# Optimization experiments

Hardware: AMD Instinct MI355X
Metric: run time of the kernel (lower is better)

## Reference

```python
import jax, jax.numpy as jnp
import numpy as np

D_MODEL, D_K, D_V, NUM_HEADS = 1024, 64, 64, 16
B, T = 4, 2048


def setup_inputs() -> dict:
    key = jax.random.key(0)
    ks = jax.random.split(key, 9)
    s = 0.02
    inp = {
        "input_Q": jax.random.normal(ks[0], (B, T, D_MODEL), dtype=jnp.float32),
        # causal mask: True = masked out (matches torch masked_fill semantics)
        "mask": jnp.triu(jnp.ones((T, T), dtype=bool), k=1),
        "Wq": jax.random.normal(ks[1], (D_MODEL, D_K * NUM_HEADS), dtype=jnp.float32) * s,
        "bq": jnp.zeros((D_K * NUM_HEADS,), dtype=jnp.float32),
        "Wk": jax.random.normal(ks[2], (D_MODEL, D_K * NUM_HEADS), dtype=jnp.float32) * s,
        "bk": jnp.zeros((D_K * NUM_HEADS,), dtype=jnp.float32),
        "Wv": jax.random.normal(ks[3], (D_MODEL, D_V * NUM_HEADS), dtype=jnp.float32) * s,
        "bv": jnp.zeros((D_V * NUM_HEADS,), dtype=jnp.float32),
        "Wo": jax.random.normal(ks[4], (D_V * NUM_HEADS, D_MODEL), dtype=jnp.float32) * s,
        "bo": jnp.zeros((D_MODEL,), dtype=jnp.float32),
    }
    return inp


def reference(input_Q, mask, Wq, bq, Wk, bk, Wv, bv, Wo, bo):
    b, t, _ = input_Q.shape
    h, dk, dv = NUM_HEADS, D_K, D_V
    # projections, then split heads: [b, t, h*d] -> [b, h, t, d]
    Q = (input_Q @ Wq + bq).reshape(b, t, h, dk).transpose(0, 2, 1, 3)
    K = (input_Q @ Wk + bk).reshape(b, t, h, dk).transpose(0, 2, 1, 3)
    V = (input_Q @ Wv + bv).reshape(b, t, h, dv).transpose(0, 2, 1, 3)
    # scaled dot-product attention with full [b, h, t, t] scores (as original)
    scores = jnp.einsum("bhqd,bhkd->bhqk", Q, K) * (1.0 / np.sqrt(dk).astype(np.float32))
    scores = jnp.where(mask, jnp.float32(-jnp.inf), scores)
    attn = jax.nn.softmax(scores, axis=-1)
    ctx = jnp.einsum("bhqk,bhkd->bhqd", attn, V)  # [b, h, t, dv]
    combined = ctx.transpose(0, 2, 1, 3).reshape(b, t, h * dv)
    return combined @ Wo + bo
```

## Files before the change

### kernel.cpp

```cpp
#include <hip/hip_runtime.h>
#include <hip/hip_bf16.h>
#include <stdint.h>

#define B_  4
#define T_  2048
#define H_  16
#define DH  64
#define DM  1024

typedef unsigned short u16;
typedef float  f32x4  __attribute__((ext_vector_type(4)));
typedef u16    u16x4  __attribute__((ext_vector_type(4)));
typedef __bf16 bf16x8 __attribute__((ext_vector_type(8)));
typedef bf16x8 __attribute__((may_alias, aligned(16))) bf16x8_a;
typedef u16x4  __attribute__((may_alias, aligned(8)))  u16x4_a;

__device__ __forceinline__ void gld16(void* lds, const void* g) {
  __builtin_amdgcn_global_load_lds((const __attribute__((address_space(1))) unsigned int*)g,
                                   (__attribute__((address_space(3))) unsigned int*)lds,
                                   16, 0, 0);
}
__device__ __forceinline__ u16 f2b(float f) {
  __bf16 h = (__bf16)f; return __builtin_bit_cast(unsigned short, h);
}

__global__ void cvt_x(const float* __restrict__ in, u16* __restrict__ out) {
  const int i = (blockIdx.x * 256 + threadIdx.x) * 4;
  const f32x4 v = *(const f32x4*)&in[i];
  u16x4 o;
  o.x = f2b(v.x); o.y = f2b(v.y); o.z = f2b(v.z); o.w = f2b(v.w);
  *(u16x4_a*)&out[i] = o;
}

__global__ void transpose4(const float* __restrict__ Wq, const float* __restrict__ Wk,
                           const float* __restrict__ Wv, const float* __restrict__ Wo,
                           u16* __restrict__ WqT, u16* __restrict__ WkT,
                           u16* __restrict__ WvT, u16* __restrict__ WoT) {
  const float* in; u16* out;
  switch (blockIdx.z) {
    case 0: in = Wq; out = WqT; break;
    case 1: in = Wk; out = WkT; break;
    case 2: in = Wv; out = WvT; break;
    default: in = Wo; out = WoT; break;
  }
  __shared__ u16 t[32][33];
  const int bx = blockIdx.x * 32, by = blockIdx.y * 32;
  const int tx = threadIdx.x & 31, ty = threadIdx.x >> 5;
  for (int i = ty; i < 32; i += 8) t[i][tx] = f2b(in[(size_t)(by + i) * DM + bx + tx]);
  __syncthreads();
  for (int i = ty; i < 32; i += 8) out[(size_t)(bx + i) * DM + by + tx] = t[tx][i];
}

__global__ void transpose_v(const u16* __restrict__ in, u16* __restrict__ out) {
  __shared__ u16 t[64][65];
  const int bh = blockIdx.y, t0 = blockIdx.x * 64;
  const int tx = threadIdx.x & 63, ty = threadIdx.x >> 6;
  const u16* ib = in  + (size_t)bh * T_ * DH;
  u16*       ob = out + (size_t)bh * DH * T_;
  for (int i = ty; i < 64; i += 4) t[i][tx] = ib[(size_t)(t0 + i) * DH + tx];
  __syncthreads();
  for (int i = ty; i < 64; i += 4) ob[(size_t)i * T_ + t0 + tx] = t[tx][i];
}

__device__ __forceinline__ void gemm_bt_128(
    const u16* __restrict__ A, const u16* __restrict__ BT,
    const float* __restrict__ bias, float oscale,
    u16* __restrict__ C, float* __restrict__ Cf, int mode)
{
  constexpr int K = 1024, N = 1024;
  __shared__ __attribute__((aligned(16))) u16 lA[128 * 32];
  __shared__ __attribute__((aligned(16))) u16 lB[128 * 32];
  const int tid  = threadIdx.x;
  const int lane = tid & 63;
  const int quad = lane >> 4, ln = lane & 15;
  const int wave = tid >> 6;
  const int wm = wave >> 1, wn = wave & 1;
  const int m0 = blockIdx.y * 128, n0 = blockIdx.x * 128;

  const f32x4 fz = {0.f, 0.f, 0.f, 0.f};
  f32x4 acc[4][4];
#pragma unroll
  for (int i = 0; i < 4; i++)
#pragma unroll
    for (int j = 0; j < 4; j++) acc[i][j] = fz;

  const int o0 = tid * 16;
  for (int k0 = 0; k0 < K; k0 += 32) {
    __syncthreads();
#pragma unroll
    for (int p = 0; p < 2; ++p) {
      const int o = p * 4096 + o0;
      const int row = o >> 6, cole = (o & 63) >> 1;
      gld16(&lA[o >> 1], &A [(size_t)(m0 + row) * K + k0 + cole]);
      gld16(&lB[o >> 1], &BT[(size_t)(n0 + row) * K + k0 + cole]);
    }
    __syncthreads();
    bf16x8 af[4], bf[4];
#pragma unroll
    for (int i = 0; i < 4; i++)
      af[i] = *(const bf16x8_a*)&lA[(wm * 64 + i * 16 + ln) * 32 + quad * 8];
#pragma unroll
    for (int j = 0; j < 4; j++)
      bf[j] = *(const bf16x8_a*)&lB[(wn * 64 + j * 16 + ln) * 32 + quad * 8];
#pragma unroll
    for (int i = 0; i < 4; i++)
#pragma unroll
      for (int j = 0; j < 4; j++)
        acc[i][j] = __builtin_amdgcn_mfma_f32_16x16x32_bf16(af[i], bf[j], acc[i][j], 0, 0, 0);
  }

#pragma unroll
  for (int j = 0; j < 4; j++) {
    const int n = n0 + wn * 64 + j * 16 + ln;
    const float bn = bias[n];
#pragma unroll
    for (int i = 0; i < 4; i++) {
      const int mb = m0 + wm * 64 + i * 16 + quad * 4;
#pragma unroll
      for (int r = 0; r < 4; r++) {
        const int m = mb + r;
        const float v = (acc[i][j][r] + bn) * oscale;
        if (mode == 0) {
          const int b = m >> 11, t = m & 2047, h = n >> 6, d = n & 63;
          C[((size_t)((b * H_ + h) * T_ + t)) * DH + d] = f2b(v);
        } else {
          Cf[(size_t)m * N + n] = v;
        }
      }
    }
  }
}

__global__ __launch_bounds__(256, 2) void qkv_gemm(
    const u16* __restrict__ X,
    const u16* __restrict__ WqT, const u16* __restrict__ WkT, const u16* __restrict__ WvT,
    const float* __restrict__ bq, const float* __restrict__ bk, const float* __restrict__ bv,
    u16* __restrict__ Qo, u16* __restrict__ Ko, u16* __restrict__ Vo)
{
  const u16 *BT; const float* bias; u16* C; float sc;
  if (blockIdx.z == 0)      { BT = WqT; bias = bq; C = Qo; sc = 0.1803368801111144f; }
  else if (blockIdx.z == 1) { BT = WkT; bias = bk; C = Ko; sc = 1.0f; }
  else                      { BT = WvT; bias = bv; C = Vo; sc = 1.0f; }
  gemm_bt_128(X, BT, bias, sc, C, nullptr, 0);
}

__global__ __launch_bounds__(256, 2) void out_gemm(
    const u16* __restrict__ ctx, const u16* __restrict__ WoT,
    const float* __restrict__ bo, float* __restrict__ out)
{
  gemm_bt_128(ctx, WoT, bo, 1.0f, nullptr, out, 2);
}

__global__ __launch_bounds__(512, 4) void flash_attn(
    const u16* __restrict__ Q, const u16* __restrict__ Kg,
    const u16* __restrict__ Vt, u16* __restrict__ ctx)
{
  __shared__ __attribute__((aligned(16))) u16 lK[128 * 64];
  __shared__ __attribute__((aligned(16))) u16 lV[64 * 128];
  __shared__ __attribute__((aligned(16))) u16 lP[128 * 64];

  const int bh = blockIdx.x;
  const int b  = bh >> 4, h = bh & 15;
  const int qi = 15 - blockIdx.y;
  const int q0 = qi * 128;
  const int tid = threadIdx.x;
  const int lane = tid & 63, wave = tid >> 6;
  const int quad = lane >> 4, ln = lane & 15;
  const int ln7 = ln & 7, ln8 = ln >> 3;
  const int w16 = wave * 16;

  const u16* Qbh = Q  + (size_t)bh * T_ * DH;
  const u16* Kbh = Kg + (size_t)bh * T_ * DH;
  const u16* Vbh = Vt + (size_t)bh * DH * T_;

#pragma unroll
  for (int p = 0; p < 2; ++p) {
    const int P = p * 512 + tid;
    const int row = P >> 3, c = (P & 7) ^ (row & 7);
    gld16(&lK[P * 8], &Qbh[(size_t)(q0 + row) * DH + c * 8]);
  }
  __syncthreads();
  bf16x8 aq[2];
#pragma unroll
  for (int ks = 0; ks < 2; ++ks)
    aq[ks] = *(const bf16x8_a*)&lK[(w16 + ln) * 64 + (((ks * 4 + quad) ^ ln7) << 3)];

  bf16x8 ones;
#pragma unroll
  for (int i = 0; i < 8; i++) ones[i] = (__bf16)1.0f;

  const f32x4 fz = {0.f, 0.f, 0.f, 0.f};
  f32x4 accO[4];
  f32x4 accL;
#pragma unroll
  for (int j = 0; j < 4; j++) accO[j] = fz;
  accL = fz;

  auto tile_step = [&](int kt, bool MASK) {
    const int t0 = kt * 128;
    __syncthreads();
#pragma unroll
    for (int p = 0; p < 2; ++p) {
      const int P = p * 512 + tid;
      const int row = P >> 3, c = (P & 7) ^ (row & 7);
      gld16(&lK[P * 8], &Kbh[(size_t)(t0 + row) * DH + c * 8]);
    }
#pragma unroll
    for (int p = 0; p < 2; ++p) {
      const int P = p * 512 + tid;
      const int row = P >> 4, c = (P & 15) ^ (row & 15);
      gld16(&lV[P * 8], &Vbh[(size_t)row * T_ + t0 + c * 8]);
    }
    __syncthreads();

#pragma unroll
    for (int half = 0; half < 2; ++half) {
      f32x4 s[4];
#pragma unroll
      for (int jj = 0; jj < 4; jj++) s[jj] = fz;
#pragma unroll
      for (int ks = 0; ks < 2; ++ks) {
        bf16x8 bk4[4];
#pragma unroll
        for (int jj = 0; jj < 4; jj++)
          bk4[jj] = *(const bf16x8_a*)&lK[((half * 4 + jj) * 16 + ln) * 64 + (((ks * 4 + quad) ^ ln7) << 3)];
#pragma unroll
        for (int jj = 0; jj < 4; jj++)
          s[jj] = __builtin_amdgcn_mfma_f32_16x16x32_bf16(aq[ks], bk4[jj], s[jj], 0, 0, 0);
      }

#pragma unroll
      for (int jj = 0; jj < 4; jj++)
#pragma unroll
        for (int r = 0; r < 4; r++) {
          float z = s[jj][r];
          if (MASK) {
            const int qrow = q0 + w16 + quad * 4 + r;
            if ((t0 + (half * 4 + jj) * 16 + ln) > qrow) z = -INFINITY;
          }
          s[jj][r] = __builtin_amdgcn_exp2f(z);
        }

#pragma unroll
      for (int jj = 0; jj < 4; jj++) {
        const int c = jj * 2 + ln8;
#pragma unroll
        for (int r = 0; r < 4; r++) {
          const int row = w16 + quad * 4 + r;
          lP[row * 64 + ((c ^ (row & 7)) << 3) + ln7] = f2b(s[jj][r]);
        }
      }

#pragma unroll
      for (int ks2 = 0; ks2 < 2; ++ks2) {
        const int ks = half * 2 + ks2;
        bf16x8 ap, bv4[4];
        ap = *(const bf16x8_a*)&lP[(w16 + ln) * 64 + (((ks2 * 4 + quad) ^ ln7) << 3)];
        accL = __builtin_amdgcn_mfma_f32_16x16x32_bf16(ap, ones, accL, 0, 0, 0);
#pragma unroll
        for (int j2 = 0; j2 < 4; j2++)
          bv4[j2] = *(const bf16x8_a*)&lV[(j2 * 16 + ln) * 128 + (((ks * 4 + quad) ^ ln) << 3)];
#pragma unroll
        for (int j2 = 0; j2 < 4; j2++)
          accO[j2] = __builtin_amdgcn_mfma_f32_16x16x32_bf16(ap, bv4[j2], accO[j2], 0, 0, 0);
      }
    }
  };

  for (int kt = 0; kt < qi; ++kt) tile_step(kt, false);
  tile_step(qi, true);

#pragma unroll
  for (int r = 0; r < 4; r++) {
    const int qrow = q0 + w16 + quad * 4 + r;
    const float inv = 1.0f / accL[r];
#pragma unroll
    for (int j2 = 0; j2 < 4; j2++) {
      const int d = j2 * 16 + ln;
      ctx[((size_t)(b * T_ + qrow)) * DM + h * DH + d] = f2b(accO[j2][r] * inv);
    }
  }
}

extern "C" void kernel_launch(void* const* d_in, const int* in_sizes, int n_in,
                              void* d_out, int out_size, void* d_ws, size_t ws_size,
                              hipStream_t stream) {
  (void)in_sizes; (void)n_in; (void)out_size; (void)ws_size;
  const float* X  = (const float*)d_in[0];
  const float* Wq = (const float*)d_in[2];
  const float* bq = (const float*)d_in[3];
  const float* Wk = (const float*)d_in[4];
  const float* bk = (const float*)d_in[5];
  const float* Wv = (const float*)d_in[6];
  const float* bv = (const float*)d_in[7];
  const float* Wo = (const float*)d_in[8];
  const float* bo = (const float*)d_in[9];
  float* out = (float*)d_out;

  char* ws = (char*)d_ws;
  u16* WqT = (u16*)(ws + (0ull  << 20));
  u16* WkT = (u16*)(ws + (2ull  << 20));
  u16* WvT = (u16*)(ws + (4ull  << 20));
  u16* WoT = (u16*)(ws + (6ull  << 20));
  u16* Xb  = (u16*)(ws + (8ull  << 20));
  u16* Qb  = (u16*)(ws + (24ull << 20));
  u16* Kb  = (u16*)(ws + (40ull << 20));
  u16* Vb  = (u16*)(ws + (56ull << 20));
  u16* Vtb = (u16*)(ws + (72ull << 20));
  u16* ctx = (u16*)(ws + (88ull << 20));

  cvt_x<<<8192, 256, 0, stream>>>(X, Xb);
  transpose4<<<dim3(32, 32, 4), 256, 0, stream>>>(Wq, Wk, Wv, Wo, WqT, WkT, WvT, WoT);
  qkv_gemm<<<dim3(8, 64, 3), 256, 0, stream>>>(Xb, WqT, WkT, WvT, bq, bk, bv, Qb, Kb, Vb);
  transpose_v<<<dim3(32, 64), 256, 0, stream>>>(Vb, Vtb);
  flash_attn<<<dim3(64, 16), 512, 0, stream>>>(Qb, Kb, Vtb, ctx);
  out_gemm<<<dim3(8, 64), 256, 0, stream>>>(ctx, WoT, bo, out);
}
```

Before: 293.3 us.

## Double GEMM K-tile with XOR-swizzled LDS and merge prep kernels

The shared GEMM helper now stages 64-wide K tiles instead of 32, which halves the number of barrier pairs per K loop. It stores the tiles in LDS with an XOR swizzle on 16-byte chunks so fragment reads avoid bank conflicts. The X conversion and the weight transposes are merged into one prep launch, removing a kernel launch. LDS use per block doubles to 32KB, which can reduce occupancy.

```diff
diff --git a/kernel.cpp b/kernel.cpp
--- a/kernel.cpp
+++ b/kernel.cpp
@@ -24,18 +24,24 @@
   __bf16 h = (__bf16)f; return __builtin_bit_cast(unsigned short, h);
 }
 
-__global__ void cvt_x(const float* __restrict__ in, u16* __restrict__ out) {
-  const int i = (blockIdx.x * 256 + threadIdx.x) * 4;
-  const f32x4 v = *(const f32x4*)&in[i];
-  u16x4 o;
-  o.x = f2b(v.x); o.y = f2b(v.y); o.z = f2b(v.z); o.w = f2b(v.w);
-  *(u16x4_a*)&out[i] = o;
-}
-
-__global__ void transpose4(const float* __restrict__ Wq, const float* __restrict__ Wk,
-                           const float* __restrict__ Wv, const float* __restrict__ Wo,
-                           u16* __restrict__ WqT, u16* __restrict__ WkT,
-                           u16* __restrict__ WvT, u16* __restrict__ WoT) {
+__global__ void prep(const float* __restrict__ X,
+                     const float* __restrict__ Wq, const float* __restrict__ Wk,
+                     const float* __restrict__ Wv, const float* __restrict__ Wo,
+                     u16* __restrict__ Xb,
+                     u16* __restrict__ WqT, u16* __restrict__ WkT,
+                     u16* __restrict__ WvT, u16* __restrict__ WoT) {
+  if (blockIdx.z == 4) {
+    const int bi = blockIdx.y * 32 + blockIdx.x;
+#pragma unroll
+    for (int p = 0; p < 8; ++p) {
+      const int i = bi * 8192 + p * 1024 + threadIdx.x * 4;
+      const f32x4 v = *(const f32x4*)&X[i];
+      u16x4 o;
+      o.x = f2b(v.x); o.y = f2b(v.y); o.z = f2b(v.z); o.w = f2b(v.w);
+      *(u16x4_a*)&Xb[i] = o;
+    }
+    return;
+  }
   const float* in; u16* out;
   switch (blockIdx.z) {
     case 0: in = Wq; out = WqT; break;
@@ -68,11 +74,12 @@
     u16* __restrict__ C, float* __restrict__ Cf, int mode)
 {
   constexpr int K = 1024, N = 1024;
-  __shared__ __attribute__((aligned(16))) u16 lA[128 * 32];
-  __shared__ __attribute__((aligned(16))) u16 lB[128 * 32];
+  __shared__ __attribute__((aligned(16))) u16 lA[128 * 64];
+  __shared__ __attribute__((aligned(16))) u16 lB[128 * 64];
   const int tid  = threadIdx.x;
   const int lane = tid & 63;
   const int quad = lane >> 4, ln = lane & 15;
+  const int ln7 = ln & 7;
   const int wave = tid >> 6;
   const int wm = wave >> 1, wn = wave & 1;
   const int m0 = blockIdx.y * 128, n0 = blockIdx.x * 128;
@@ -84,29 +91,31 @@
 #pragma unroll
     for (int j = 0; j < 4; j++) acc[i][j] = fz;
 
-  const int o0 = tid * 16;
-  for (int k0 = 0; k0 < K; k0 += 32) {
+  for (int k0 = 0; k0 < K; k0 += 64) {
     __syncthreads();
 #pragma unroll
-    for (int p = 0; p < 2; ++p) {
-      const int o = p * 4096 + o0;
-      const int row = o >> 6, cole = (o & 63) >> 1;
-      gld16(&lA[o >> 1], &A [(size_t)(m0 + row) * K + k0 + cole]);
-      gld16(&lB[o >> 1], &BT[(size_t)(n0 + row) * K + k0 + cole]);
+    for (int p = 0; p < 4; ++p) {
+      const int P = p * 256 + tid;
+      const int row = P >> 3, c = (P & 7) ^ (row & 7);
+      gld16(&lA[P * 8], &A [(size_t)(m0 + row) * K + k0 + c * 8]);
+      gld16(&lB[P * 8], &BT[(size_t)(n0 + row) * K + k0 + c * 8]);
     }
     __syncthreads();
-    bf16x8 af[4], bf[4];
-#pragma unroll
-    for (int i = 0; i < 4; i++)
-      af[i] = *(const bf16x8_a*)&lA[(wm * 64 + i * 16 + ln) * 32 + quad * 8];
-#pragma unroll
-    for (int j = 0; j < 4; j++)
-      bf[j] = *(const bf16x8_a*)&lB[(wn * 64 + j * 16 + ln) * 32 + quad * 8];
-#pragma unroll
-    for (int i = 0; i < 4; i++)
+#pragma unroll
+    for (int ks = 0; ks < 2; ++ks) {
+      bf16x8 af[4], bf[4];
+#pragma unroll
+      for (int i = 0; i < 4; i++)
+        af[i] = *(const bf16x8_a*)&lA[(wm * 64 + i * 16 + ln) * 64 + (((ks * 4 + quad) ^ ln7) << 3)];
 #pragma unroll
       for (int j = 0; j < 4; j++)
-        acc[i][j] = __builtin_amdgcn_mfma_f32_16x16x32_bf16(af[i], bf[j], acc[i][j], 0, 0, 0);
+        bf[j] = *(const bf16x8_a*)&lB[(wn * 64 + j * 16 + ln) * 64 + (((ks * 4 + quad) ^ ln7) << 3)];
+#pragma unroll
+      for (int i = 0; i < 4; i++)
+#pragma unroll
+        for (int j = 0; j < 4; j++)
+          acc[i][j] = __builtin_amdgcn_mfma_f32_16x16x32_bf16(af[i], bf[j], acc[i][j], 0, 0, 0);
+    }
   }
 
 #pragma unroll
@@ -309,8 +318,7 @@
   u16* Vtb = (u16*)(ws + (72ull << 20));
   u16* ctx = (u16*)(ws + (88ull << 20));
 
-  cvt_x<<<8192, 256, 0, stream>>>(X, Xb);
-  transpose4<<<dim3(32, 32, 4), 256, 0, stream>>>(Wq, Wk, Wv, Wo, WqT, WkT, WvT, WoT);
+  prep<<<dim3(32, 32, 5), 256, 0, stream>>>(X, Wq, Wk, Wv, Wo, Xb, WqT, WkT, WvT, WoT);
   qkv_gemm<<<dim3(8, 64, 3), 256, 0, stream>>>(Xb, WqT, WkT, WvT, bq, bk, bv, Qb, Kb, Vb);
   transpose_v<<<dim3(32, 64), 256, 0, stream>>>(Vb, Vtb);
   flash_attn<<<dim3(64, 16), 512, 0, stream>>>(Qb, Kb, Vtb, ctx);
```

After: 275.5 us. 6.1% less time.
